# Performance work log

Hardware: AMD Instinct MI355X
Metric: run time of the kernel (lower is better)

## Reference

```python
import jax, jax.numpy as jnp
import numpy as np

B, C, M = 8192, 1024, 4096  # batch, controller width, memory_size


def setup_inputs() -> dict:
    key = jax.random.key(0)
    k1, k2, k3 = jax.random.split(key, 3)
    memory = jax.random.normal(k1, (B, M), dtype=jnp.float32)
    controller_output = jax.random.normal(k2, (B, C), dtype=jnp.float32)
    W = jax.random.normal(k3, (C, M), dtype=jnp.float32) * 0.02  # Dense kernel
    b = jnp.zeros((M,), dtype=jnp.float32)                       # Dense bias
    return {"memory": memory, "controller_output": controller_output, "W": W, "b": b}


def _l2_normalize(x, eps=1e-12):
    # matches tf.linalg.l2_normalize: x / sqrt(max(sum(x^2), eps))
    return x / jnp.sqrt(jnp.maximum(jnp.sum(x * x, axis=-1, keepdims=True), eps))


def reference(memory, controller_output, W, b):
    # Dense key projection followed by softmax over memory width
    key_vec = jax.nn.softmax(controller_output @ W + b, axis=-1)        # [B, M]
    # tf.keras.losses.cosine_similarity = -sum(l2n(a) * l2n(b), -1)
    sims = -jnp.sum(_l2_normalize(key_vec) * _l2_normalize(memory), axis=-1)  # [B]
    read_weights = jax.nn.softmax(sims, axis=-1)                        # softmax over B (as in source)
    read_vector = jnp.sum(read_weights[:, None] * memory, axis=1)       # [B]
    return read_vector
```

## Files before the change

### kernel.cpp

```cpp
#include <hip/hip_runtime.h>

#define NB 8192
#define NC 1024
#define NM 4096
#define NCH 64

typedef __attribute__((ext_vector_type(8))) short bf16x8;
typedef __attribute__((ext_vector_type(4))) float f32x4;

__device__ __forceinline__ unsigned short f2bf(float x) {
  unsigned int u = __float_as_uint(x);
  u += 0x7FFFu + ((u >> 16) & 1u);
  return (unsigned short)(u >> 16);
}
__device__ __forceinline__ unsigned int pk2(float a, float b) {
  return (unsigned int)f2bf(a) | ((unsigned int)f2bf(b) << 16);
}

__device__ __forceinline__ void gload_lds16(const void* g, void* l) {
  __builtin_amdgcn_global_load_lds(
      (const __attribute__((address_space(1))) unsigned int*)g,
      (__attribute__((address_space(3))) unsigned int*)l, 16, 0, 0);
}

__global__ __launch_bounds__(256) void convA_k(const float* __restrict__ src,
                                               unsigned short* __restrict__ dst) {
  const size_t i = ((size_t)blockIdx.x * 256 + threadIdx.x) * 8;
  const float4* s = reinterpret_cast<const float4*>(src + i);
  float4 x0 = s[0], x1 = s[1];
  int4 o = make_int4((int)pk2(x0.x, x0.y), (int)pk2(x0.z, x0.w),
                     (int)pk2(x1.x, x1.y), (int)pk2(x1.z, x1.w));
  *reinterpret_cast<int4*>(dst + i) = o;
}

__global__ __launch_bounds__(256) void convW_k(const float* __restrict__ W,
                                               unsigned short* __restrict__ Wt) {
  __shared__ float tile[64][65];
  const int n0 = blockIdx.x * 64, k0 = blockIdx.y * 64;
  const int t = threadIdx.x;
  const int r = t >> 2, q = t & 3;
  const float4* src = reinterpret_cast<const float4*>(W + (size_t)(k0 + r) * NM + n0 + q * 16);
  float4 x0 = src[0], x1 = src[1], x2 = src[2], x3 = src[3];
  float* tr = &tile[r][q * 16];
  tr[0]=x0.x; tr[1]=x0.y; tr[2]=x0.z;  tr[3]=x0.w;
  tr[4]=x1.x; tr[5]=x1.y; tr[6]=x1.z;  tr[7]=x1.w;
  tr[8]=x2.x; tr[9]=x2.y; tr[10]=x2.z; tr[11]=x2.w;
  tr[12]=x3.x; tr[13]=x3.y; tr[14]=x3.z; tr[15]=x3.w;
  __syncthreads();
  unsigned int pk[8];
#pragma unroll
  for (int i = 0; i < 8; ++i)
    pk[i] = pk2(tile[q * 16 + 2 * i][r], tile[q * 16 + 2 * i + 1][r]);
  int4* dst = reinterpret_cast<int4*>(Wt + (size_t)(n0 + r) * NC + k0 + q * 16);
  dst[0] = make_int4((int)pk[0], (int)pk[1], (int)pk[2], (int)pk[3]);
  dst[1] = make_int4((int)pk[4], (int)pk[5], (int)pk[6], (int)pk[7]);
}

__global__ __launch_bounds__(512) void gemm_fused(
    const unsigned short* __restrict__ Abf, const float* __restrict__ memry,
    const unsigned short* __restrict__ Wt, const float* __restrict__ bvec,
    float* __restrict__ pdotg, float* __restrict__ pesqg,
    float* __restrict__ pmsqg, float* __restrict__ pmsg) {
  __shared__ __align__(16) unsigned short LDS[2][4][8192];
  const int bm = blockIdx.x, bn = blockIdx.y;
  const int row0 = bm * 256, col0 = bn * 256;
  const int t = threadIdx.x;
  const int wid = t >> 6, lane = t & 63;
  const int wr = wid >> 2, wc = wid & 3;
  const int l15 = lane & 15, lg = lane >> 4;
  const int ga8 = (lg ^ ((l15 >> 1) & 3)) * 8;

  f32x4 acc[8][4];
#pragma unroll
  for (int mi = 0; mi < 8; ++mi)
#pragma unroll
    for (int ni = 0; ni < 4; ++ni) acc[mi][ni] = (f32x4){0.f, 0.f, 0.f, 0.f};

  const int srow0 = t >> 2;
  const int sk8 = ((t & 3) ^ ((srow0 >> 1) & 3)) * 8;
  const unsigned short* gA = Abf + (size_t)(row0 + srow0) * NC + sk8;
  const unsigned short* gB = Wt + (size_t)(col0 + srow0) * NC + sk8;

#define STG(SL, TY, KT)                                                      \
  {                                                                          \
    const unsigned short* s0 = ((TY) <= 1 ? gA : gB) + (KT) * 64 + ((TY)&1) * 32; \
    gload_lds16(s0, &LDS[SL][TY][t * 8]);                                    \
    gload_lds16(s0 + (size_t)128 * NC, &LDS[SL][TY][t * 8 + 4096]);          \
  }
#define NOSTG
#define VM6 asm volatile("s_waitcnt vmcnt(6)" ::: "memory")
#define VM0 asm volatile("s_waitcnt vmcnt(0)" ::: "memory")
#define NOVM

#define PH(SL, S, MH, RDB, STAGE, VM)                                        \
  {                                                                          \
    if (RDB) {                                                               \
      _Pragma("unroll") for (int ni = 0; ni < 4; ++ni)                       \
          b[ni] = *reinterpret_cast<const bf16x8*>(                          \
              &LDS[SL][2 + (S)][(wc * 64 + ni * 16 + l15) * 32 + ga8]);      \
    }                                                                        \
    _Pragma("unroll") for (int mi = 0; mi < 4; ++mi)                         \
        a[mi] = *reinterpret_cast<const bf16x8*>(                            \
            &LDS[SL][S][(wr * 128 + (MH)*64 + mi * 16 + l15) * 32 + ga8]);   \
    STAGE;                                                                   \
    VM;                                                                      \
    __builtin_amdgcn_s_barrier();                                            \
    __builtin_amdgcn_sched_barrier(0);                                       \
    __builtin_amdgcn_s_setprio(1);                                           \
    _Pragma("unroll") for (int mi = 0; mi < 4; ++mi)                         \
        _Pragma("unroll") for (int ni = 0; ni < 4; ++ni)                     \
            acc[(MH)*4 + mi][ni] = __builtin_amdgcn_mfma_f32_16x16x32_bf16(  \
                a[mi], b[ni], acc[(MH)*4 + mi][ni], 0, 0, 0);                \
    __builtin_amdgcn_s_setprio(0);                                           \
    __builtin_amdgcn_s_barrier();                                            \
    __builtin_amdgcn_sched_barrier(0);                                       \
  }

  STG(0, 2, 0); STG(0, 0, 0); STG(0, 3, 0); STG(0, 1, 0);
  STG(1, 2, 1); STG(1, 0, 1); STG(1, 3, 1);
  VM6;
  __builtin_amdgcn_s_barrier();
  __builtin_amdgcn_sched_barrier(0);

  bf16x8 a[4], b[4];
  for (int it = 0; it < 7; ++it) {
    const int c1 = 2 * it + 1, c2 = 2 * it + 2, c3 = 2 * it + 3;
    PH(0, 0, 0, true,  STG(1, 1, c1), NOVM);
    PH(0, 0, 1, false, STG(0, 2, c2), NOVM);
    PH(0, 1, 0, true,  STG(0, 0, c2), NOVM);
    PH(0, 1, 1, false, STG(0, 3, c2), VM6);
    PH(1, 0, 0, true,  STG(0, 1, c2), NOVM);
    PH(1, 0, 1, false, STG(1, 2, c3), NOVM);
    PH(1, 1, 0, true,  STG(1, 0, c3), NOVM);
    PH(1, 1, 1, false, STG(1, 3, c3), VM6);
  }
  PH(0, 0, 0, true,  STG(1, 1, 15), NOVM);
  PH(0, 0, 1, false, NOSTG, NOVM);
  PH(0, 1, 0, true,  NOSTG, NOVM);
  PH(0, 1, 1, false, NOSTG, VM0);
  PH(1, 0, 0, true,  NOSTG, NOVM);
  PH(1, 0, 1, false, NOSTG, NOVM);
  PH(1, 1, 0, true,  NOSTG, NOVM);
  PH(1, 1, 1, false, NOSTG, NOVM);
#undef PH
#undef STG

  float bv[4];
#pragma unroll
  for (int ni = 0; ni < 4; ++ni) bv[ni] = bvec[col0 + wc * 64 + ni * 16 + l15];

  const int chunk = bn * 4 + wc;
#pragma unroll
  for (int mi = 0; mi < 8; ++mi) {
#pragma unroll
    for (int j = 0; j < 4; ++j) {
      const int rowm = row0 + wr * 128 + mi * 16 + 4 * lg + j;
      float pd = 0.f, pe = 0.f, pq = 0.f, pm = 0.f;
#pragma unroll
      for (int ni = 0; ni < 4; ++ni) {
        float e = __expf(acc[mi][ni][j] + bv[ni]);
        float mv = memry[(size_t)rowm * NM + col0 + wc * 64 + ni * 16 + l15];
        pd += e * mv; pe += e * e; pq += mv * mv; pm += mv;
      }
#pragma unroll
      for (int s = 1; s < 16; s <<= 1) {
        pd += __shfl_xor(pd, s);
        pe += __shfl_xor(pe, s);
        pq += __shfl_xor(pq, s);
        pm += __shfl_xor(pm, s);
      }
      if (l15 == 0) {
        const int idx = rowm * NCH + chunk;
        pdotg[idx] = pd; pesqg[idx] = pe; pmsqg[idx] = pq; pmsg[idx] = pm;
      }
    }
  }
}

__global__ __launch_bounds__(256) void finalize_k(
    const float* __restrict__ pd, const float* __restrict__ pe,
    const float* __restrict__ pq, const float* __restrict__ pm,
    float* __restrict__ sims, float* __restrict__ mst) {
  const int r = blockIdx.x * 256 + threadIdx.x;
  float d = 0.f, e = 0.f, q = 0.f, m = 0.f;
#pragma unroll
  for (int i = 0; i < NCH; ++i) {
    d += pd[r * NCH + i];
    e += pe[r * NCH + i];
    q += pq[r * NCH + i];
    m += pm[r * NCH + i];
  }
  sims[r] = -d / (sqrtf(fmaxf(e, 1e-12f)) * sqrtf(fmaxf(q, 1e-12f)));
  mst[r] = m;
}

__global__ __launch_bounds__(1024) void softmax_out_k(
    const float* __restrict__ sims, const float* __restrict__ mst,
    float* __restrict__ out) {
  __shared__ float red[16];
  const int t = threadIdx.x;
  float v[8];
  float mx = -1e30f;
#pragma unroll
  for (int i = 0; i < 8; ++i) {
    v[i] = sims[t + i * 1024];
    mx = fmaxf(mx, v[i]);
  }
#pragma unroll
  for (int s = 1; s < 64; s <<= 1) mx = fmaxf(mx, __shfl_xor(mx, s));
  if ((t & 63) == 0) red[t >> 6] = mx;
  __syncthreads();
  float m2 = red[0];
#pragma unroll
  for (int i = 1; i < 16; ++i) m2 = fmaxf(m2, red[i]);
  mx = m2;
  float sum = 0.f;
#pragma unroll
  for (int i = 0; i < 8; ++i) sum += __expf(v[i] - mx);
#pragma unroll
  for (int s = 1; s < 64; s <<= 1) sum += __shfl_xor(sum, s);
  __syncthreads();
  if ((t & 63) == 0) red[t >> 6] = sum;
  __syncthreads();
  float s2 = 0.f;
#pragma unroll
  for (int i = 0; i < 16; ++i) s2 += red[i];
  const float inv = 1.0f / s2;
#pragma unroll
  for (int i = 0; i < 8; ++i)
    out[t + i * 1024] = __expf(v[i] - mx) * inv * mst[t + i * 1024];
}

extern "C" void kernel_launch(void* const* d_in, const int* in_sizes, int n_in,
                              void* d_out, int out_size, void* d_ws, size_t ws_size,
                              hipStream_t stream) {
  const float* memry = (const float*)d_in[0];
  const float* co    = (const float*)d_in[1];
  const float* W     = (const float*)d_in[2];
  const float* bvec  = (const float*)d_in[3];
  float* out = (float*)d_out;

  char* w = (char*)d_ws;
  unsigned short* Wt  = (unsigned short*)w;
  unsigned short* Abf = Wt + (size_t)NM * NC;
  float* pdot = (float*)(Abf + (size_t)NB * NC);
  float* pesq = pdot + (size_t)NB * NCH;
  float* pmsq = pesq + (size_t)NB * NCH;
  float* pms  = pmsq + (size_t)NB * NCH;
  float* sims = pms  + (size_t)NB * NCH;
  float* mst  = sims + NB;

  convA_k<<<(size_t)NB * NC / (256 * 8), 256, 0, stream>>>(co, Abf);
  convW_k<<<dim3(NM / 64, NC / 64), 256, 0, stream>>>(W, Wt);
  gemm_fused<<<dim3(NB / 256, NM / 256), 512, 0, stream>>>(Abf, memry, Wt, bvec,
                                                           pdot, pesq, pmsq, pms);
  finalize_k<<<NB / 256, 256, 0, stream>>>(pdot, pesq, pmsq, pms, sims, mst);
  softmax_out_k<<<1, 1024, 0, stream>>>(sims, mst, out);
}
```

Baseline: 126.6 us.

## Stage exp tile in LDS as bf16 for coalesced row-wise epilogue reduction

The GEMM epilogue now writes exp(acc+bias) to LDS as bf16, then re-reads it row-wise so each half-wave reads 8 contiguous floats of memory per lane with vector loads. Per-block partials are reduced across the full 256-column tile, which drops the number of partial chunks per row from 64 to 16 and shrinks the finalize pass's reads. The aim is to replace strided scalar memory reads and many small partial writes with coalesced loads and fewer outputs. In exchange it adds an LDS round-trip and a __syncthreads, and it rounds e to bf16 before the dot and squared-norm sums, which lowers accuracy.

```diff
diff --git a/kernel.cpp b/kernel.cpp
--- a/kernel.cpp
+++ b/kernel.cpp
@@ -3,7 +3,7 @@
 #define NB 8192
 #define NC 1024
 #define NM 4096
-#define NCH 64
+#define NCH 16
 
 typedef __attribute__((ext_vector_type(8))) short bf16x8;
 typedef __attribute__((ext_vector_type(4))) float f32x4;
@@ -145,32 +145,46 @@
 #undef PH
 #undef STG
 
+  unsigned short (*e_lds)[256] = reinterpret_cast<unsigned short(*)[256]>(&LDS[0][0][0]);
   float bv[4];
 #pragma unroll
   for (int ni = 0; ni < 4; ++ni) bv[ni] = bvec[col0 + wc * 64 + ni * 16 + l15];
-
-  const int chunk = bn * 4 + wc;
-#pragma unroll
-  for (int mi = 0; mi < 8; ++mi) {
-#pragma unroll
-    for (int j = 0; j < 4; ++j) {
-      const int rowm = row0 + wr * 128 + mi * 16 + 4 * lg + j;
+#pragma unroll
+  for (int mi = 0; mi < 8; ++mi)
+#pragma unroll
+    for (int ni = 0; ni < 4; ++ni)
+#pragma unroll
+      for (int j = 0; j < 4; ++j) {
+        const int rl = wr * 128 + mi * 16 + 4 * lg + j;
+        const int cl = wc * 64 + ni * 16 + l15;
+        e_lds[rl][cl] = f2bf(__expf(acc[mi][ni][j] + bv[ni]));
+      }
+  __syncthreads();
+
+  {
+    const int halfl = lane >> 5, l31 = lane & 31;
+    const int rbase = wid * 32;
+#pragma unroll 4
+    for (int i = 0; i < 16; ++i) {
+      const int rl = rbase + 2 * i + halfl;
+      const float4* mp = reinterpret_cast<const float4*>(
+          memry + (size_t)(row0 + rl) * NM + col0 + l31 * 8);
+      float4 m0 = mp[0], m1 = mp[1];
+      bf16x8 ev = *reinterpret_cast<const bf16x8*>(&e_lds[rl][l31 * 8]);
+      float mv[8] = {m0.x, m0.y, m0.z, m0.w, m1.x, m1.y, m1.z, m1.w};
       float pd = 0.f, pe = 0.f, pq = 0.f, pm = 0.f;
 #pragma unroll
-      for (int ni = 0; ni < 4; ++ni) {
-        float e = __expf(acc[mi][ni][j] + bv[ni]);
-        float mv = memry[(size_t)rowm * NM + col0 + wc * 64 + ni * 16 + l15];
-        pd += e * mv; pe += e * e; pq += mv * mv; pm += mv;
-      }
-#pragma unroll
-      for (int s = 1; s < 16; s <<= 1) {
-        pd += __shfl_xor(pd, s);
-        pe += __shfl_xor(pe, s);
-        pq += __shfl_xor(pq, s);
-        pm += __shfl_xor(pm, s);
-      }
-      if (l15 == 0) {
-        const int idx = rowm * NCH + chunk;
+      for (int k = 0; k < 8; ++k) {
+        float e = __uint_as_float(((unsigned int)(unsigned short)ev[k]) << 16);
+        pd += e * mv[k]; pe += e * e; pq += mv[k] * mv[k]; pm += mv[k];
+      }
+#pragma unroll
+      for (int s = 1; s < 32; s <<= 1) {
+        pd += __shfl_xor(pd, s); pe += __shfl_xor(pe, s);
+        pq += __shfl_xor(pq, s); pm += __shfl_xor(pm, s);
+      }
+      if (l31 == 0) {
+        const int idx = (row0 + rl) * NCH + bn;
         pdotg[idx] = pd; pesqg[idx] = pe; pmsqg[idx] = pq; pmsg[idx] = pm;
       }
     }
```

New measurement: 109.3 us. 1.16x faster.
